# Performance work log

Measured on AMD Instinct MI355X. Metric: run time of the kernel, lower is better.

## Reference

```python
import jax, jax.numpy as jnp
import numpy as np

N = 4096          # num_nodes
U = 2048          # num_users
R = 5             # num_relations
B = 30            # num_bases
H0 = 500          # hidden_size[0]
H1 = 75           # hidden_size[1]
E = 262144        # num_edges
EPS = 1e-5


def setup_inputs() -> dict:
    key = jax.random.key(0)
    ks = jax.random.split(key, 10)
    x = jax.random.normal(ks[0], (N, N), dtype=jnp.float32)
    edge_index = jax.random.randint(ks[1], (2, E), 0, N, dtype=jnp.int64)
    edge_type = jax.random.randint(ks[2], (E,), 0, R, dtype=jnp.int64)
    # RGCNConv basis-decomposition parameters
    basis = jax.random.normal(ks[3], (B, N, H0), dtype=jnp.float32) * 0.02
    comp = jax.random.normal(ks[4], (R, B), dtype=jnp.float32) * 0.1
    root = jax.random.normal(ks[5], (N, H0), dtype=jnp.float32) * 0.02
    bias_rgcn = jnp.zeros((H0,), dtype=jnp.float32)
    # DenseLayer (Linear without bias) + BatchNorm1d affine params
    fc_w = jax.random.normal(ks[6], (H1, H0), dtype=jnp.float32) * 0.05
    bn_gamma_u = jnp.ones((U,), dtype=jnp.float32)
    bn_beta_u = jnp.zeros((U,), dtype=jnp.float32)
    bn_gamma_i = jnp.ones((N - U,), dtype=jnp.float32)
    bn_beta_i = jnp.zeros((N - U,), dtype=jnp.float32)
    return {
        "x": x, "basis": basis, "comp": comp, "root": root,
        "bias_rgcn": bias_rgcn, "fc_w": fc_w,
        "bn_gamma_u": bn_gamma_u, "bn_beta_u": bn_beta_u,
        "bn_gamma_i": bn_gamma_i, "bn_beta_i": bn_beta_i,
        "edge_index": edge_index, "edge_type": edge_type,
    }


def _bn1d(z, gamma, beta):
    # BatchNorm1d applied to z.unsqueeze(0): channels = rows, normalize over feature dim
    mu = z.mean(axis=1, keepdims=True)
    var = ((z - mu) ** 2).mean(axis=1, keepdims=True)
    return gamma[:, None] * (z - mu) / jnp.sqrt(var + EPS) + beta[:, None]


def _forward(x, basis, comp, root, bias_rgcn, fc_w,
             bn_gamma_u, bn_beta_u, bn_gamma_i, bn_beta_i,
             edge_index, edge_type):
    # --- RGCNConv with basis decomposition, mean aggregation per relation ---
    W = jnp.einsum('rb,bio->rio', comp, basis)          # [R, N, H0]
    h = jnp.einsum('ni,rio->rno', x, W)                 # [R, N, H0] transformed feats
    src, dst = edge_index[0], edge_index[1]
    msgs = h[edge_type, src]                            # [E, H0] gather
    seg = dst * R + edge_type                           # (target, relation) segments
    sums = jax.ops.segment_sum(msgs, seg, num_segments=N * R)
    cnt = jax.ops.segment_sum(jnp.ones((E,), dtype=msgs.dtype), seg, num_segments=N * R)
    agg = (sums / jnp.maximum(cnt, 1.0)[:, None]).reshape(N, R, H0).sum(axis=1)
    feats = agg + x @ root + bias_rgcn                  # [N, H0]

    # --- separate (accum != 'stack') ---
    u, i = feats[:U], feats[U:]

    # --- DenseLayer: dropout (eval: identity) -> Linear(no bias) -> BN -> ReLU ---
    u = jax.nn.relu(_bn1d(u @ fc_w.T, bn_gamma_u, bn_beta_u))
    i = jax.nn.relu(_bn1d(i @ fc_w.T, bn_gamma_i, bn_beta_i))
    return u, i


def reference(x, basis, comp, root, bias_rgcn, fc_w,
              bn_gamma_u, bn_beta_u, bn_gamma_i, bn_beta_i,
              edge_index, edge_type):
    return _forward(x, basis, comp, root, bias_rgcn, fc_w,
                    bn_gamma_u, bn_beta_u, bn_gamma_i, bn_beta_i,
                    edge_index, edge_type)
```

## Files before the change

kernel.cpp:

```cpp
#include <hip/hip_runtime.h>
#include <hip/hip_bf16.h>
#include <stdint.h>

#define N_NODES 4096
#define U_NODES 2048
#define R_REL 5
#define B_BASES 30
#define H0 500
#define H1 75
#define E_EDGES 262144
#define EPS_BN 1e-5f
#define K_DIM 4096
#define M_COLS 3000
#define M_PAD 3072
#define NSEG (N_NODES*R_REL)

typedef __attribute__((ext_vector_type(4))) float f32x4;
typedef __attribute__((ext_vector_type(8))) short bf16x8;

static __device__ __forceinline__ ushort bf16_bits(float f) {
    union { float f; uint32_t u; } c; c.f = f;
    uint32_t u = c.u;
    uint32_t r = (u + 0x7fffu + ((u >> 16) & 1u)) >> 16;
    return (ushort)r;
}

static __device__ __forceinline__ float bf16_to_f(ushort u) {
    union { uint32_t u; float f; } c; c.u = ((uint32_t)u) << 16; return c.f;
}

static __device__ __forceinline__ void fma_u4(f32x4& s, float w, ushort4 v) {
    s.x += w * bf16_to_f(v.x); s.y += w * bf16_to_f(v.y);
    s.z += w * bf16_to_f(v.z); s.w += w * bf16_to_f(v.w);
}

static __device__ __forceinline__ void async_copy16(const ushort* g, ushort* l) {
    __builtin_amdgcn_global_load_lds((const __attribute__((address_space(1))) void*)g,
                                     (__attribute__((address_space(3))) void*)l,
                                     16, 0, 0);
}

__global__ void k_convert_x(const float* __restrict__ x, ushort* __restrict__ xb,
                            int* __restrict__ cnt) {
    int gid = blockIdx.x * 256 + threadIdx.x;
    if (gid < NSEG) cnt[gid] = 0;
    int i = gid * 4;
    float4 v = *(const float4*)(x + i);
    ushort4 o;
    o.x = bf16_bits(v.x); o.y = bf16_bits(v.y);
    o.z = bf16_bits(v.z); o.w = bf16_bits(v.w);
    *(ushort4*)(xb + i) = o;
}

__global__ void k_make_wallT(const float* __restrict__ basis, const float* __restrict__ comp,
                             const float* __restrict__ root, ushort* __restrict__ wallT) {
    __shared__ float compl_[R_REL * B_BASES];
    __shared__ float T[32][33];
    int t = threadIdx.x;
    if (t < R_REL * B_BASES) compl_[t] = comp[t];
    __syncthreads();
    int k0 = blockIdx.x * 32, o0 = blockIdx.y * 32;
    int o_in = t & 31, k_in = t >> 5;
    int o = o0 + o_in;
    bool ov = (o < H0);
    float acc[4][6];
    #pragma unroll
    for (int a = 0; a < 4; a++)
        #pragma unroll
        for (int r = 0; r < 6; r++) acc[a][r] = 0.f;
    for (int b = 0; b < B_BASES; b++) {
        float cw[5];
        #pragma unroll
        for (int r = 0; r < 5; r++) cw[r] = compl_[r * B_BASES + b];
        #pragma unroll
        for (int a = 0; a < 4; a++) {
            int k = k0 + a * 8 + k_in;
            float v = ov ? basis[(size_t)b * K_DIM * H0 + (size_t)k * H0 + o] : 0.f;
            #pragma unroll
            for (int r = 0; r < 5; r++) acc[a][r] += cw[r] * v;
        }
    }
    #pragma unroll
    for (int a = 0; a < 4; a++) {
        int k = k0 + a * 8 + k_in;
        acc[a][5] = ov ? root[(size_t)k * H0 + o] : 0.f;
    }
    for (int r = 0; r < 6; r++) {
        __syncthreads();
        #pragma unroll
        for (int a = 0; a < 4; a++) T[o_in][a * 8 + k_in] = acc[a][r];
        __syncthreads();
        int ro = t >> 5, ck = t & 31;
        #pragma unroll
        for (int a = 0; a < 4; a++) {
            int oo = ro + a * 8;
            int om = o0 + oo;
            if (om < H0) {
                int m = r * H0 + om;
                wallT[(size_t)m * K_DIM + k0 + ck] = bf16_bits(T[oo][ck]);
            }
        }
    }
}

__global__ __launch_bounds__(256) void k_gemm(const ushort* __restrict__ A,
                                              const ushort* __restrict__ BT,
                                              ushort* __restrict__ C) {
    __shared__ __align__(16) ushort As[128 * 64];
    __shared__ __align__(16) ushort Bs[128 * 64];
    int tid = threadIdx.x;
    int lane = tid & 63, wave = tid >> 6;
    int bid = blockIdx.x;
    int xcd = bid & 7;
    int j = bid >> 3;
    int n_t = xcd * 3 + (j >> 5);
    int m_t = j & 31;
    int m0 = m_t * 128, n0 = n_t * 128;
    int wm = (wave & 1) * 64, wn = (wave >> 1) * 64;

    f32x4 acc[4][4];
    #pragma unroll
    for (int a = 0; a < 4; a++)
        #pragma unroll
        for (int b = 0; b < 4; b++) { f32x4 z = {0.f, 0.f, 0.f, 0.f}; acc[a][b] = z; }

    int srow = tid >> 3;
    int skc = (((tid & 7) ^ ((tid >> 3) & 7))) * 8;
    const ushort* Abase = A + (size_t)(m0 + srow) * K_DIM + skc;
    const ushort* Bbase = BT + (size_t)(n0 + srow) * K_DIM + skc;
    int ldsoff = (wave * 64) * 8;

    for (int k0 = 0; k0 < K_DIM; k0 += 64) {
        const ushort* ga = Abase + k0;
        const ushort* gb = Bbase + k0;
        #pragma unroll
        for (int i = 0; i < 4; i++) {
            async_copy16(ga + (size_t)i * 32 * K_DIM, As + i * 2048 + ldsoff);
            async_copy16(gb + (size_t)i * 32 * K_DIM, Bs + i * 2048 + ldsoff);
        }
        __syncthreads();
        #pragma unroll
        for (int kk = 0; kk < 64; kk += 32) {
            bf16x8 af[4], bfr[4];
            int koff = kk + ((lane >> 4) * 8);
            int g = koff >> 3;
            #pragma unroll
            for (int a = 0; a < 4; a++) {
                int row = wm + a * 16 + (lane & 15);
                int sw = (g ^ (row & 7)) * 8;
                af[a] = *(const bf16x8*)(As + row * 64 + sw);
            }
            #pragma unroll
            for (int b = 0; b < 4; b++) {
                int row = wn + b * 16 + (lane & 15);
                int sw = (g ^ (row & 7)) * 8;
                bfr[b] = *(const bf16x8*)(Bs + row * 64 + sw);
            }
            #pragma unroll
            for (int a = 0; a < 4; a++)
                #pragma unroll
                for (int b = 0; b < 4; b++)
                    acc[a][b] = __builtin_amdgcn_mfma_f32_16x16x32_bf16(af[a], bfr[b], acc[a][b], 0, 0, 0);
        }
        __syncthreads();
    }

    int col = lane & 15;
    int rbase = (lane >> 4) * 4;
    #pragma unroll
    for (int a = 0; a < 4; a++) {
        #pragma unroll
        for (int b = 0; b < 4; b++) {
            int gn = n0 + wn + b * 16 + col;
            if (gn < M_COLS) {
                #pragma unroll
                for (int r = 0; r < 4; r++) {
                    int gm = m0 + wm + a * 16 + rbase + r;
                    C[(size_t)gm * M_COLS + gn] = bf16_bits(acc[a][b][r]);
                }
            }
        }
    }
}

__global__ void k_count(const int* __restrict__ ei, const int* __restrict__ et, int* __restrict__ cnt) {
    int e = blockIdx.x * 256 + threadIdx.x;
    if (e < E_EDGES) {
        int dst = ei[E_EDGES + e];
        int r = et[e];
        atomicAdd(&cnt[dst * R_REL + r], 1);
    }
}

__global__ void k_scan(const int* __restrict__ cnt, int* __restrict__ offs, int* __restrict__ cursor) {
    __shared__ int part[256];
    int t = threadIdx.x;
    int4 buf[20];
    const int4* c4 = (const int4*)(cnt + t * 80);
    int s = 0;
    #pragma unroll
    for (int i = 0; i < 20; i++) { buf[i] = c4[i]; s += buf[i].x + buf[i].y + buf[i].z + buf[i].w; }
    part[t] = s;
    __syncthreads();
    for (int d = 1; d < 256; d <<= 1) {
        int v = (t >= d) ? part[t - d] : 0;
        __syncthreads();
        part[t] += v;
        __syncthreads();
    }
    int run = part[t] - s;
    int4* o4 = (int4*)(offs + t * 80);
    int4* u4 = (int4*)(cursor + t * 80);
    #pragma unroll
    for (int i = 0; i < 20; i++) {
        int4 c = buf[i];
        int4 o;
        o.x = run; o.y = run + c.x; o.z = run + c.x + c.y; o.w = run + c.x + c.y + c.z;
        run += c.x + c.y + c.z + c.w;
        o4[i] = o; u4[i] = o;
    }
    if (t == 255) offs[NSEG] = run;
}

__global__ void k_fill(const int* __restrict__ ei, const int* __restrict__ et,
                       const int* __restrict__ offs, int* __restrict__ cursor,
                       int* __restrict__ edge_val, float* __restrict__ edge_w) {
    int e = blockIdx.x * 256 + threadIdx.x;
    if (e < E_EDGES) {
        int src = ei[e];
        int dst = ei[E_EDGES + e];
        int r = et[e];
        int seg = dst * R_REL + r;
        int pos = atomicAdd(&cursor[seg], 1);
        edge_val[pos] = (src << 3) | r;
        edge_w[pos] = 1.0f / (float)(offs[seg + 1] - offs[seg]);
    }
}

__global__ void k_agg(const ushort* __restrict__ C, const int* __restrict__ offs,
                      const int* __restrict__ edge_val, const float* __restrict__ edge_w,
                      const float* __restrict__ bias, float* __restrict__ feats) {
    int n = blockIdx.x;
    int t = threadIdx.x;
    if (t >= 125) return;
    int beg = offs[n * R_REL];
    int end = offs[n * R_REL + R_REL];
    f32x4 s0 = {0.f,0.f,0.f,0.f}, s1 = {0.f,0.f,0.f,0.f};
    f32x4 s2 = {0.f,0.f,0.f,0.f}, s3 = {0.f,0.f,0.f,0.f};
    const ushort* Ct = C + t * 4;
    int e = beg;
    for (; e + 3 < end; e += 4) {
        int   v0 = edge_val[e],   v1 = edge_val[e+1], v2 = edge_val[e+2], v3 = edge_val[e+3];
        float w0 = edge_w[e],     w1 = edge_w[e+1],   w2 = edge_w[e+2],   w3 = edge_w[e+3];
        ushort4 a0 = *(const ushort4*)(Ct + (size_t)(v0 >> 3) * M_COLS + (v0 & 7) * H0);
        ushort4 a1 = *(const ushort4*)(Ct + (size_t)(v1 >> 3) * M_COLS + (v1 & 7) * H0);
        ushort4 a2 = *(const ushort4*)(Ct + (size_t)(v2 >> 3) * M_COLS + (v2 & 7) * H0);
        ushort4 a3 = *(const ushort4*)(Ct + (size_t)(v3 >> 3) * M_COLS + (v3 & 7) * H0);
        fma_u4(s0, w0, a0); fma_u4(s1, w1, a1); fma_u4(s2, w2, a2); fma_u4(s3, w3, a3);
    }
    for (; e < end; e++) {
        int v = edge_val[e];
        float w = edge_w[e];
        ushort4 a = *(const ushort4*)(Ct + (size_t)(v >> 3) * M_COLS + (v & 7) * H0);
        fma_u4(s0, w, a);
    }
    f32x4 acc = (s0 + s1) + (s2 + s3);
    {
        ushort4 v = *(const ushort4*)(C + (size_t)n * M_COLS + 5 * H0 + t * 4);
        acc.x += bf16_to_f(v.x); acc.y += bf16_to_f(v.y);
        acc.z += bf16_to_f(v.z); acc.w += bf16_to_f(v.w);
    }
    acc += *(const f32x4*)(bias + t * 4);
    *(f32x4*)(feats + (size_t)n * H0 + t * 4) = acc;
}

__global__ __launch_bounds__(128) void k_fc_bn(const float* __restrict__ feats, const float* __restrict__ fcw,
                                               const float* __restrict__ gu, const float* __restrict__ bu,
                                               const float* __restrict__ gi, const float* __restrict__ bi,
                                               float* __restrict__ out) {
    __shared__ float fs[4][H0];
    __shared__ float z[4][80];
    int t = threadIdx.x;
    int row0 = blockIdx.x * 4;
    if (t < 125) {
        #pragma unroll
        for (int r = 0; r < 4; r++)
            *(f32x4*)&fs[r][t * 4] = *(const f32x4*)(feats + (size_t)(row0 + r) * H0 + t * 4);
    }
    __syncthreads();
    if (t < H1) {
        float a0 = 0.f, a1 = 0.f, a2 = 0.f, a3 = 0.f;
        const float* wr = fcw + (size_t)t * H0;
        for (int k = 0; k < H0; k += 4) {
            float4 w = *(const float4*)(wr + k);
            a0 += w.x * fs[0][k] + w.y * fs[0][k+1] + w.z * fs[0][k+2] + w.w * fs[0][k+3];
            a1 += w.x * fs[1][k] + w.y * fs[1][k+1] + w.z * fs[1][k+2] + w.w * fs[1][k+3];
            a2 += w.x * fs[2][k] + w.y * fs[2][k+1] + w.z * fs[2][k+2] + w.w * fs[2][k+3];
            a3 += w.x * fs[3][k] + w.y * fs[3][k+1] + w.z * fs[3][k+2] + w.w * fs[3][k+3];
        }
        z[0][t] = a0; z[1][t] = a1; z[2][t] = a2; z[3][t] = a3;
    }
    __syncthreads();
    int lane = t & 63, wave = t >> 6;
    #pragma unroll
    for (int rr = 0; rr < 2; rr++) {
        int r = wave * 2 + rr;
        int row = row0 + r;
        float a = (lane < H1) ? z[r][lane] : 0.f;
        float b2 = (lane < H1 - 64) ? z[r][64 + lane] : 0.f;
        float s1 = a + b2, s2 = a * a + b2 * b2;
        #pragma unroll
        for (int s = 32; s > 0; s >>= 1) { s1 += __shfl_xor(s1, s); s2 += __shfl_xor(s2, s); }
        float mean = s1 / (float)H1;
        float var = s2 / (float)H1 - mean * mean;
        float inv = 1.0f / sqrtf(var + EPS_BN);
        float gamma, beta;
        if (row < U_NODES) { gamma = gu[row];            beta = bu[row]; }
        else               { gamma = gi[row - U_NODES];  beta = bi[row - U_NODES]; }
        if (lane < H1) {
            float v = gamma * (a - mean) * inv + beta;
            out[(size_t)row * H1 + lane] = v > 0.f ? v : 0.f;
        }
        if (lane < H1 - 64) {
            float v = gamma * (b2 - mean) * inv + beta;
            out[(size_t)row * H1 + 64 + lane] = v > 0.f ? v : 0.f;
        }
    }
}

extern "C" void kernel_launch(void* const* d_in, const int* in_sizes, int n_in,
                              void* d_out, int out_size, void* d_ws, size_t ws_size,
                              hipStream_t stream) {
    (void)in_sizes; (void)n_in; (void)out_size; (void)ws_size;
    const float* x         = (const float*)d_in[0];
    const float* basis     = (const float*)d_in[1];
    const float* comp      = (const float*)d_in[2];
    const float* root      = (const float*)d_in[3];
    const float* bias_rgcn = (const float*)d_in[4];
    const float* fc_w      = (const float*)d_in[5];
    const float* gu        = (const float*)d_in[6];
    const float* bu        = (const float*)d_in[7];
    const float* gi        = (const float*)d_in[8];
    const float* bi        = (const float*)d_in[9];
    const int*   ei        = (const int*)d_in[10];
    const int*   et        = (const int*)d_in[11];
    float* out = (float*)d_out;

    char* ws = (char*)d_ws;
    size_t off = 0;
    auto carve = [&](size_t bytes) -> void* {
        void* p = ws + off;
        off += (bytes + 255) & ~(size_t)255;
        return p;
    };
    ushort* xb      = (ushort*)carve((size_t)N_NODES * K_DIM * 2);
    ushort* wallT   = (ushort*)carve((size_t)M_PAD * K_DIM * 2);
    ushort* hall    = (ushort*)carve((size_t)N_NODES * M_COLS * 2);
    float*  feats   = (float*) carve((size_t)N_NODES * H0 * 4);
    int*    cnt     = (int*)   carve((size_t)NSEG * 4);
    int*    offs    = (int*)   carve((size_t)(NSEG + 1) * 4);
    int*    cursor  = (int*)   carve((size_t)NSEG * 4);
    int*    edge_val= (int*)   carve((size_t)E_EDGES * 4);
    float*  edge_w  = (float*) carve((size_t)E_EDGES * 4);

    k_convert_x<<<16384, 256, 0, stream>>>(x, xb, cnt);
    k_make_wallT<<<dim3(128, 16), 256, 0, stream>>>(basis, comp, root, wallT);
    k_count<<<E_EDGES / 256, 256, 0, stream>>>(ei, et, cnt);
    k_scan<<<1, 256, 0, stream>>>(cnt, offs, cursor);
    k_fill<<<E_EDGES / 256, 256, 0, stream>>>(ei, et, offs, cursor, edge_val, edge_w);
    k_gemm<<<768, 256, 0, stream>>>(xb, wallT, hall);
    k_agg<<<N_NODES, 128, 0, stream>>>(hall, offs, edge_val, edge_w, bias_rgcn, feats);
    k_fc_bn<<<N_NODES / 4, 128, 0, stream>>>(feats, fc_w, gu, bu, gi, bi, out);
}
```

Measured before the change: 622.2 us.

## Rewrite GEMM as 256x256 double-buffered 8-wave pipeline with staged async loads

The bf16 GEMM moves from 128x128 tiles with 4 waves and a single-buffered LDS to 256x256 tiles with 8 waves and double-buffered LDS. Global-to-LDS async copies for the next K tile are split into quarters and interleaved with four MFMA phases, using fine-grained barriers, vmcnt waits and s_setprio. The aim is to hide memory latency behind MFMA work and raise data reuse per tile. The cost is more LDS and registers per block and only 192 blocks, which leaves some CUs idle and adds tail effects on the 3000-column padded edge.

```diff
diff --git a/kernel.cpp b/kernel.cpp
--- a/kernel.cpp
+++ b/kernel.cpp
@@ -103,80 +103,162 @@
     }
 }
 
-__global__ __launch_bounds__(256) void k_gemm(const ushort* __restrict__ A,
-                                              const ushort* __restrict__ BT,
-                                              ushort* __restrict__ C) {
-    __shared__ __align__(16) ushort As[128 * 64];
-    __shared__ __align__(16) ushort Bs[128 * 64];
-    int tid = threadIdx.x;
-    int lane = tid & 63, wave = tid >> 6;
+__global__ __launch_bounds__(512, 2) void k_gemm(const ushort* __restrict__ A,
+                                                 const ushort* __restrict__ BT,
+                                                 ushort* __restrict__ C) {
+    __shared__ __align__(16) ushort lds[65536];
+    const int tid  = threadIdx.x;
+    const int lane = tid & 63;
+    const int wave = tid >> 6;
     int bid = blockIdx.x;
-    int xcd = bid & 7;
-    int j = bid >> 3;
-    int n_t = xcd * 3 + (j >> 5);
-    int m_t = j & 31;
-    int m0 = m_t * 128, n0 = n_t * 128;
-    int wm = (wave & 1) * 64, wn = (wave >> 1) * 64;
-
-    f32x4 acc[4][4];
-    #pragma unroll
-    for (int a = 0; a < 4; a++)
-        #pragma unroll
-        for (int b = 0; b < 4; b++) { f32x4 z = {0.f, 0.f, 0.f, 0.f}; acc[a][b] = z; }
-
-    int srow = tid >> 3;
-    int skc = (((tid & 7) ^ ((tid >> 3) & 7))) * 8;
-    const ushort* Abase = A + (size_t)(m0 + srow) * K_DIM + skc;
-    const ushort* Bbase = BT + (size_t)(n0 + srow) * K_DIM + skc;
-    int ldsoff = (wave * 64) * 8;
-
-    for (int k0 = 0; k0 < K_DIM; k0 += 64) {
-        const ushort* ga = Abase + k0;
-        const ushort* gb = Bbase + k0;
-        #pragma unroll
-        for (int i = 0; i < 4; i++) {
-            async_copy16(ga + (size_t)i * 32 * K_DIM, As + i * 2048 + ldsoff);
-            async_copy16(gb + (size_t)i * 32 * K_DIM, Bs + i * 2048 + ldsoff);
-        }
-        __syncthreads();
-        #pragma unroll
-        for (int kk = 0; kk < 64; kk += 32) {
-            bf16x8 af[4], bfr[4];
-            int koff = kk + ((lane >> 4) * 8);
-            int g = koff >> 3;
+    int wg  = (bid & 7) * 24 + (bid >> 3);
+    const int m0 = (wg & 15) << 8;
+    const int n0 = (wg >> 4) << 8;
+    const int wm = (wave >> 2) << 7;
+    const int wn = (wave & 3) << 6;
+
+    const int sj = tid >> 3;
+    const int sc = tid & 7;
+    const int sg = sc ^ (sj & 7);
+
+    const ushort* Ab = A  + (size_t)m0 * K_DIM + (size_t)sg * 8;
+    const ushort* Bb = BT + (size_t)n0 * K_DIM + (size_t)sg * 8;
+
+    f32x4 acc[8][4];
+    #pragma unroll
+    for (int i = 0; i < 8; i++)
+        #pragma unroll
+        for (int j = 0; j < 4; j++) { f32x4 z = {0.f,0.f,0.f,0.f}; acc[i][j] = z; }
+
+    auto stageA = [&](int pb, int h, int Tn) {
+        #pragma unroll
+        for (int i = 0; i < 2; i++) {
+            const ushort* src = Ab + (size_t)(h * 64 + sj + 128 * i) * K_DIM + Tn * 64;
+            ushort* dst = lds + pb * 16384 + h * 4096 + (wave << 9) + i * 8192;
+            async_copy16(src, dst);
+        }
+    };
+    auto stageB = [&](int pb, int h, int Tn) {
+        #pragma unroll
+        for (int i = 0; i < 2; i++) {
+            int comb = sj + 64 * i;
+            const ushort* src = Bb + (size_t)((comb >> 5) * 64 + h * 32 + (comb & 31)) * K_DIM + Tn * 64;
+            int cb = (wave << 3) + 64 * i;
+            ushort* dst = lds + 32768 + pb * 16384 + ((cb >> 5) << 12) + (h << 11) + ((cb & 31) << 6);
+            async_copy16(src, dst);
+        }
+    };
+    auto readA = [&](int pb, int fm, int s) -> bf16x8 {
+        int row = wm + fm * 16 + (lane & 15);
+        int ch  = (s * 4 + (lane >> 4)) ^ (row & 7);
+        return *(const bf16x8*)(lds + pb * 16384 + row * 64 + ch * 8);
+    };
+    auto readB = [&](int pb, int fn, int s) -> bf16x8 {
+        int row = wn + fn * 16 + (lane & 15);
+        int ch  = (s * 4 + (lane >> 4)) ^ (row & 7);
+        return *(const bf16x8*)(lds + 32768 + pb * 16384 + row * 64 + ch * 8);
+    };
+
+    stageA(0, 0, 0); stageB(0, 0, 0); stageB(0, 1, 0); stageA(0, 1, 0);
+    asm volatile("s_waitcnt vmcnt(2)" ::: "memory");
+    __builtin_amdgcn_s_barrier();
+    asm volatile("" ::: "memory");
+
+    bf16x8 a[4][2], b[4][2];
+
+    for (int T = 0; T < 64; T++) {
+        int pb = T & 1, qb = pb ^ 1;
+        int Tn = (T + 1) & 63;
+
+        #pragma unroll
+        for (int fm = 0; fm < 4; fm++) { a[fm][0] = readA(pb, fm, 0); a[fm][1] = readA(pb, fm, 1); }
+        #pragma unroll
+        for (int fn = 0; fn < 2; fn++) { b[fn][0] = readB(pb, fn, 0); b[fn][1] = readB(pb, fn, 1); }
+        stageA(qb, 0, Tn);
+        asm volatile("" ::: "memory");
+        __builtin_amdgcn_s_barrier();
+        asm volatile("" ::: "memory");
+        __builtin_amdgcn_s_setprio(1);
+        #pragma unroll
+        for (int fm = 0; fm < 4; fm++)
             #pragma unroll
-            for (int a = 0; a < 4; a++) {
-                int row = wm + a * 16 + (lane & 15);
-                int sw = (g ^ (row & 7)) * 8;
-                af[a] = *(const bf16x8*)(As + row * 64 + sw);
-            }
+            for (int fn = 0; fn < 2; fn++) {
+                acc[fm][fn] = __builtin_amdgcn_mfma_f32_16x16x32_bf16(a[fm][0], b[fn][0], acc[fm][fn], 0, 0, 0);
+                acc[fm][fn] = __builtin_amdgcn_mfma_f32_16x16x32_bf16(a[fm][1], b[fn][1], acc[fm][fn], 0, 0, 0);
+            }
+        __builtin_amdgcn_s_setprio(0);
+        asm volatile("" ::: "memory");
+        __builtin_amdgcn_s_barrier();
+        asm volatile("" ::: "memory");
+
+        #pragma unroll
+        for (int fn = 2; fn < 4; fn++) { b[fn][0] = readB(pb, fn, 0); b[fn][1] = readB(pb, fn, 1); }
+        stageB(qb, 0, Tn);
+        asm volatile("s_waitcnt vmcnt(4)" ::: "memory");
+        __builtin_amdgcn_s_barrier();
+        asm volatile("" ::: "memory");
+        __builtin_amdgcn_s_setprio(1);
+        #pragma unroll
+        for (int fm = 0; fm < 4; fm++)
             #pragma unroll
-            for (int b = 0; b < 4; b++) {
-                int row = wn + b * 16 + (lane & 15);
-                int sw = (g ^ (row & 7)) * 8;
-                bfr[b] = *(const bf16x8*)(Bs + row * 64 + sw);
-            }
+            for (int fn = 2; fn < 4; fn++) {
+                acc[fm][fn] = __builtin_amdgcn_mfma_f32_16x16x32_bf16(a[fm][0], b[fn][0], acc[fm][fn], 0, 0, 0);
+                acc[fm][fn] = __builtin_amdgcn_mfma_f32_16x16x32_bf16(a[fm][1], b[fn][1], acc[fm][fn], 0, 0, 0);
+            }
+        __builtin_amdgcn_s_setprio(0);
+        asm volatile("" ::: "memory");
+        __builtin_amdgcn_s_barrier();
+        asm volatile("" ::: "memory");
+
+        #pragma unroll
+        for (int fm = 0; fm < 4; fm++) { a[fm][0] = readA(pb, 4 + fm, 0); a[fm][1] = readA(pb, 4 + fm, 1); }
+        stageB(qb, 1, Tn);
+        asm volatile("" ::: "memory");
+        __builtin_amdgcn_s_barrier();
+        asm volatile("" ::: "memory");
+        __builtin_amdgcn_s_setprio(1);
+        #pragma unroll
+        for (int fm = 0; fm < 4; fm++)
             #pragma unroll
-            for (int a = 0; a < 4; a++)
-                #pragma unroll
-                for (int b = 0; b < 4; b++)
-                    acc[a][b] = __builtin_amdgcn_mfma_f32_16x16x32_bf16(af[a], bfr[b], acc[a][b], 0, 0, 0);
-        }
-        __syncthreads();
-    }
-
-    int col = lane & 15;
-    int rbase = (lane >> 4) * 4;
-    #pragma unroll
-    for (int a = 0; a < 4; a++) {
-        #pragma unroll
-        for (int b = 0; b < 4; b++) {
-            int gn = n0 + wn + b * 16 + col;
+            for (int fn = 2; fn < 4; fn++) {
+                acc[4 + fm][fn] = __builtin_amdgcn_mfma_f32_16x16x32_bf16(a[fm][0], b[fn][0], acc[4 + fm][fn], 0, 0, 0);
+                acc[4 + fm][fn] = __builtin_amdgcn_mfma_f32_16x16x32_bf16(a[fm][1], b[fn][1], acc[4 + fm][fn], 0, 0, 0);
+            }
+        __builtin_amdgcn_s_setprio(0);
+        asm volatile("" ::: "memory");
+        __builtin_amdgcn_s_barrier();
+        asm volatile("" ::: "memory");
+
+        stageA(qb, 1, Tn);
+        asm volatile("s_waitcnt vmcnt(2)" ::: "memory");
+        __builtin_amdgcn_s_barrier();
+        asm volatile("" ::: "memory");
+        __builtin_amdgcn_s_setprio(1);
+        #pragma unroll
+        for (int fm = 0; fm < 4; fm++)
+            #pragma unroll
+            for (int fn = 0; fn < 2; fn++) {
+                acc[4 + fm][fn] = __builtin_amdgcn_mfma_f32_16x16x32_bf16(a[fm][0], b[fn][0], acc[4 + fm][fn], 0, 0, 0);
+                acc[4 + fm][fn] = __builtin_amdgcn_mfma_f32_16x16x32_bf16(a[fm][1], b[fn][1], acc[4 + fm][fn], 0, 0, 0);
+            }
+        __builtin_amdgcn_s_setprio(0);
+        asm volatile("" ::: "memory");
+        __builtin_amdgcn_s_barrier();
+        asm volatile("" ::: "memory");
+    }
+
+    const int col = lane & 15;
+    const int rbase = (lane >> 4) * 4;
+    #pragma unroll
+    for (int fm = 0; fm < 8; fm++) {
+        #pragma unroll
+        for (int fn = 0; fn < 4; fn++) {
+            int gn = n0 + wn + fn * 16 + col;
             if (gn < M_COLS) {
                 #pragma unroll
                 for (int r = 0; r < 4; r++) {
-                    int gm = m0 + wm + a * 16 + rbase + r;
-                    C[(size_t)gm * M_COLS + gn] = bf16_bits(acc[a][b][r]);
+                    int gm = m0 + wm + fm * 16 + rbase + r;
+                    C[(size_t)gm * M_COLS + gn] = bf16_bits(acc[fm][fn][r]);
                 }
             }
         }
@@ -368,7 +450,7 @@
     k_count<<<E_EDGES / 256, 256, 0, stream>>>(ei, et, cnt);
     k_scan<<<1, 256, 0, stream>>>(cnt, offs, cursor);
     k_fill<<<E_EDGES / 256, 256, 0, stream>>>(ei, et, offs, cursor, edge_val, edge_w);
-    k_gemm<<<768, 256, 0, stream>>>(xb, wallT, hall);
+    k_gemm<<<192, 512, 0, stream>>>(xb, wallT, hall);
     k_agg<<<N_NODES, 128, 0, stream>>>(hall, offs, edge_val, edge_w, bias_rgcn, feats);
     k_fc_bn<<<N_NODES / 4, 128, 0, stream>>>(feats, fc_w, gu, bu, gi, bi, out);
 }
```

Measured after the change: 645.4 us. 3.7% more time.
